# Kernel optimization log

Measured on AMD Instinct MI355X. Metric: run time of the kernel, lower is better.

The kernel has to match this reference:

```python
import math
import jax, jax.numpy as jnp
import numpy as np

H = 4            # num_attention_heads
EPS = 1e-5       # InstanceNorm / LayerNorm eps (torch default)


def _inorm(x):
    # nn.InstanceNorm1d applied to (N, S, d): normalizes over the last dim per (item, token), no affine
    m = jnp.mean(x, axis=-1, keepdims=True)
    v = jnp.var(x, axis=-1, keepdims=True)
    return (x - m) / jnp.sqrt(v + EPS)


def _tree_layer(x, Wqkv, bqkv, Wo, bo, W1, b1, W2, b2):
    # x: (N, S, d) with S=2
    N, S, d = x.shape
    dh = d // H
    qkv = x @ Wqkv.T + bqkv                      # (N, S, 3d)
    q, k, v = jnp.split(qkv, 3, axis=-1)
    q = q.reshape(N, S, H, dh)
    k = k.reshape(N, S, H, dh)
    v = v.reshape(N, S, H, dh)
    scores = jnp.einsum('nqhd,nkhd->nhqk', q, k) / math.sqrt(dh)
    att = jax.nn.softmax(scores, axis=-1)
    o = jnp.einsum('nhqk,nkhd->nqhd', att, v).reshape(N, S, d)
    o = o @ Wo.T + bo
    x = _inorm(x + o)
    f = jax.nn.gelu(x @ W1.T + b1, approximate=False) @ W2.T + b2
    return _inorm(x + f)


def _mlp(x, Wa, ba, Wb, bb):
    return jax.nn.gelu(x @ Wa.T + ba, approximate=False) @ Wb.T + bb


def setup_inputs() -> dict:
    key = jax.random.key(0)
    ks = jax.random.split(key, 16)
    B, G, d, ff, L, c = 64, 1024, 256, 1024, 4, 128
    s = 0.02
    r = lambda i, shape: (jax.random.normal(ks[i], shape, jnp.float32) * s)
    return dict(
        children=jax.random.normal(ks[0], (B, G, 2, d), jnp.float32),
        roles=r(1, (3, d)),
        Wqkv=r(2, (L, 3 * d, d)), bqkv=jnp.zeros((L, 3 * d), jnp.float32),
        Wo=r(3, (L, d, d)), bo=jnp.zeros((L, d), jnp.float32),
        W1=r(4, (L, ff, d)), b1=jnp.zeros((L, ff), jnp.float32),
        W2=r(5, (L, d, ff)), b2=jnp.zeros((L, d), jnp.float32),
        Wl1=r(6, (d, d)), bl1=jnp.zeros(d, jnp.float32),
        Wl2=r(7, (c, d)), bl2=jnp.zeros(c, jnp.float32),
        Wr1=r(8, (d, d)), br1=jnp.zeros(d, jnp.float32),
        Wr2=r(9, (c, d)), br2=jnp.zeros(c, jnp.float32),
        ln_g=jnp.ones(d, jnp.float32), ln_b=jnp.zeros(d, jnp.float32),
    )


def reference(children, roles, Wqkv, bqkv, Wo, bo, W1, b1, W2, b2,
              Wl1, bl1, Wl2, bl2, Wr1, br1, Wr2, br2, ln_g, ln_b):
    B, G, _, d = children.shape
    c = Wl2.shape[0]
    L = Wqkv.shape[0]
    # flatten (batch, group) and add inside role embeddings (rows 0,1)
    x = children.reshape(B * G, 2, d) + roles[:2][None, :, :]
    for i in range(L):
        x = _tree_layer(x, Wqkv[i], bqkv[i], Wo[i], bo[i], W1[i], b1[i], W2[i], b2[i])
    out = x.reshape(B, G, 2, d)
    left_const = _mlp(out[:, :, 0, :], Wl1, bl1, Wl2, bl2)   # (B, G, c)
    right_const = _mlp(out[:, :, 1, :], Wr1, br1, Wr2, br2)  # (B, G, c)
    mat_scores = jnp.sum(left_const * right_const, axis=-1) / math.sqrt(c)
    # LayerNorm over last dim of summed children
    s = out.sum(axis=2)
    m = jnp.mean(s, axis=-1, keepdims=True)
    v = jnp.var(s, axis=-1, keepdims=True)
    src = (s - m) / jnp.sqrt(v + EPS) * ln_g + ln_b
    return mat_scores, src
```

## Files before the change

### kernel.cpp

```cpp
#include <hip/hip_runtime.h>
#include <math.h>

#define NLAYER 4
#define DMODEL 256
#define ITEMS  32
#define MROWS  64
#define XS     264
#define BS     520
#define EPSV   1e-5f

typedef __attribute__((ext_vector_type(8))) short short8;
typedef __attribute__((ext_vector_type(4))) float f32x4;

#define OFF_WQKV 0
#define OFF_WO   786432
#define OFF_W1   1048576
#define OFF_W2   2097152
#define OFF_WL1  3145728
#define OFF_WL2  3211264
#define OFF_WR1  3244032
#define OFF_WR2  3309568
#define WS_ELEMS 3342336

static __device__ __forceinline__ float b2f(short s) {
  return __uint_as_float(((unsigned)(unsigned short)s) << 16);
}
static __device__ __forceinline__ short f2bf(float f) {
  unsigned u = __float_as_uint(f);
  return (short)((u + 0x7fffu + ((u >> 16) & 1u)) >> 16);
}
static __device__ __forceinline__ float gelu_f(float x) {
  return 0.5f * x * (1.0f + erff(x * 0.70710678118654752f));
}

template<int MT>
static __device__ void gemm_lds(const short* A, int as, int rmul, int radd,
                                const short* __restrict__ W,
                                const float* __restrict__ bias,
                                short* Out, int oc0, int oro,
                                int N, int act, int tid)
{
  const int wave = tid >> 6;
  const int lane = tid & 63;
  const int lm = lane & 15;
  const int q  = lane >> 4;
  const int ntiles = N >> 4;
  const f32x4 z = {0.f, 0.f, 0.f, 0.f};
  for (int nb = wave * 2; nb < ntiles; nb += 16) {
    f32x4 acc[MT][2];
    #pragma unroll
    for (int mt = 0; mt < MT; ++mt) { acc[mt][0] = z; acc[mt][1] = z; }
    #pragma unroll 4
    for (int kt = 0; kt < 256; kt += 32) {
      short8 b0 = *(const short8*)(W + ((nb    ) * 16 + lm) * 256 + kt + q * 8);
      short8 b1 = *(const short8*)(W + ((nb + 1) * 16 + lm) * 256 + kt + q * 8);
      #pragma unroll
      for (int mt = 0; mt < MT; ++mt) {
        short8 a = *(const short8*)(A + (rmul * (mt * 16 + lm) + radd) * as + kt + q * 8);
        acc[mt][0] = __builtin_amdgcn_mfma_f32_16x16x32_bf16(a, b0, acc[mt][0], 0, 0, 0);
        acc[mt][1] = __builtin_amdgcn_mfma_f32_16x16x32_bf16(a, b1, acc[mt][1], 0, 0, 0);
      }
    }
    #pragma unroll
    for (int mt = 0; mt < MT; ++mt) {
      #pragma unroll
      for (int nt = 0; nt < 2; ++nt) {
        int col = (nb + nt) * 16 + lm;
        float bv = bias[col];
        #pragma unroll
        for (int r = 0; r < 4; ++r) {
          float v = acc[mt][nt][r] + bv;
          if (act) v = gelu_f(v);
          Out[(oro + mt * 16 + q * 4 + r) * BS + oc0 + col] = f2bf(v);
        }
      }
    }
  }
}

static __device__ void gemm_acc512(f32x4 acc[4][2], const short* A,
                                   const short* __restrict__ W, int wc0, int tid)
{
  const int wave = tid >> 6, lane = tid & 63;
  const int lm = lane & 15, q = lane >> 4;
  #pragma unroll 2
  for (int kt = 0; kt < 512; kt += 32) {
    short8 b[2];
    #pragma unroll
    for (int nt = 0; nt < 2; ++nt)
      b[nt] = *(const short8*)(W + (wave * 32 + nt * 16 + lm) * 1024 + wc0 + kt + q * 8);
    #pragma unroll
    for (int mt = 0; mt < 4; ++mt) {
      short8 a = *(const short8*)(A + (mt * 16 + lm) * BS + kt + q * 8);
      #pragma unroll
      for (int nt = 0; nt < 2; ++nt)
        acc[mt][nt] = __builtin_amdgcn_mfma_f32_16x16x32_bf16(a, b[nt], acc[mt][nt], 0, 0, 0);
    }
  }
}

static __device__ void inorm_pass(short* Xs_, const short* Bf_, bool addx, int tid)
{
  if (tid >= MROWS * 4) return;
  int r = tid >> 2, sub = tid & 3;
  const short* bp = Bf_ + r * BS + sub * 64;
  short* xp = Xs_ + r * XS + sub * 64;
  float sum = 0.f, sq = 0.f;
  for (int e = 0; e < 64; ++e) {
    float v = b2f(bp[e]);
    if (addx) v += b2f(xp[e]);
    sum += v; sq += v * v;
  }
  sum += __shfl_xor(sum, 1); sq += __shfl_xor(sq, 1);
  sum += __shfl_xor(sum, 2); sq += __shfl_xor(sq, 2);
  float mean = sum * (1.f / 256.f);
  float rstd = rsqrtf(sq * (1.f / 256.f) - mean * mean + EPSV);
  for (int e = 0; e < 64; ++e) {
    float v = b2f(bp[e]);
    if (addx) v += b2f(xp[e]);
    xp[e] = f2bf((v - mean) * rstd);
  }
}

struct PrepArgs {
  const float* src[8];
  int n[8];
  int off[8];
};

__global__ void prep_weights(PrepArgs pa, short* __restrict__ dst, int total)
{
  int idx = blockIdx.x * 256 + threadIdx.x;
  if (idx >= total) return;
  int j = 0, off = idx;
  while (j < 7 && off >= pa.n[j]) { off -= pa.n[j]; ++j; }
  dst[pa.off[j] + off] = f2bf(pa.src[j][off]);
}

__global__ __launch_bounds__(512, 2)
void fused_encoder(const float* __restrict__ children,
                   const float* __restrict__ roles,
                   const short* __restrict__ ws,
                   const float* __restrict__ g_bqkv,
                   const float* __restrict__ g_bo,
                   const float* __restrict__ g_b1,
                   const float* __restrict__ g_b2,
                   const float* __restrict__ g_bl1, const float* __restrict__ g_bl2,
                   const float* __restrict__ g_br1, const float* __restrict__ g_br2,
                   const float* __restrict__ g_lng, const float* __restrict__ g_lnb,
                   float* __restrict__ out)
{
  __shared__ __align__(16) short Xs[MROWS * XS];
  __shared__ __align__(16) short Bf[MROWS * BS];
  __shared__ float Att[ITEMS * 16];

  const int tid = threadIdx.x;
  const int bid = blockIdx.x;

  {
    const float* src = children + (long)bid * MROWS * DMODEL;
    for (int e = tid * 4; e < MROWS * DMODEL; e += 2048) {
      int row = e >> 8, col = e & 255;
      float4 v = *(const float4*)(src + e);
      const float* rl = roles + (row & 1) * DMODEL + col;
      short* xp = Xs + row * XS + col;
      xp[0] = f2bf(v.x + rl[0]);
      xp[1] = f2bf(v.y + rl[1]);
      xp[2] = f2bf(v.z + rl[2]);
      xp[3] = f2bf(v.w + rl[3]);
    }
  }
  __syncthreads();

  for (int l = 0; l < NLAYER; ++l) {
    const short* Wqkv = ws + OFF_WQKV + l * 768 * 256;
    const short* Wo   = ws + OFF_WO   + l * 256 * 256;
    const short* W1   = ws + OFF_W1   + l * 1024 * 256;
    const short* W2   = ws + OFF_W2   + l * 256 * 1024;

    gemm_lds<4>(Xs, XS, 1, 0, Wqkv, g_bqkv + l * 768, Bf, 0, 0, 512, 0, tid);
    __syncthreads();

    if (tid < ITEMS * 8) {
      int i = tid >> 3, h = (tid >> 1) & 3, tk = tid & 1;
      const short* qp = Bf + (2 * i + tk) * BS + h * 64;
      const short* k0 = Bf + (2 * i    ) * BS + 256 + h * 64;
      const short* k1 = Bf + (2 * i + 1) * BS + 256 + h * 64;
      float s0 = 0.f, s1 = 0.f;
      for (int e = 0; e < 64; ++e) {
        float qv = b2f(qp[e]);
        s0 += qv * b2f(k0[e]);
        s1 += qv * b2f(k1[e]);
      }
      s0 *= 0.125f; s1 *= 0.125f;
      float mx = fmaxf(s0, s1);
      float e0 = __expf(s0 - mx), e1 = __expf(s1 - mx);
      float inv = 1.f / (e0 + e1);
      float* ap = Att + ((i * 4 + h) * 2 + tk) * 2;
      ap[0] = e0 * inv; ap[1] = e1 * inv;
    }
    __syncthreads();

    gemm_lds<4>(Xs, XS, 1, 0, Wqkv + 512 * 256, g_bqkv + l * 768 + 512, Bf, 0, 0, 256, 0, tid);
    __syncthreads();

    if (tid < MROWS * 4) {
      int r = tid >> 2, h = tid & 3;
      int i = r >> 1, tk = r & 1;
      const float* ap = Att + ((i * 4 + h) * 2 + tk) * 2;
      float a0 = ap[0], a1 = ap[1];
      const short* v0 = Bf + (2 * i) * BS + h * 64;
      const short* v1 = Bf + (2 * i + 1) * BS + h * 64;
      short* op = Bf + r * BS + 256 + h * 64;
      for (int e = 0; e < 64; ++e)
        op[e] = f2bf(a0 * b2f(v0[e]) + a1 * b2f(v1[e]));
    }
    __syncthreads();

    gemm_lds<4>(Bf + 256, BS, 1, 0, Wo, g_bo + l * 256, Bf, 0, 0, 256, 0, tid);
    __syncthreads();
    inorm_pass(Xs, Bf, true, tid);
    __syncthreads();

    f32x4 facc[4][2];
    {
      const f32x4 z = {0.f, 0.f, 0.f, 0.f};
      #pragma unroll
      for (int mt = 0; mt < 4; ++mt) { facc[mt][0] = z; facc[mt][1] = z; }
    }
    for (int ch = 0; ch < 2; ++ch) {
      gemm_lds<4>(Xs, XS, 1, 0, W1 + ch * 512 * 256, g_b1 + l * 1024 + ch * 512,
                  Bf, 0, 0, 512, 1, tid);
      __syncthreads();
      gemm_acc512(facc, Bf, W2, ch * 512, tid);
      __syncthreads();
    }
    {
      const int wave = tid >> 6, lane = tid & 63, lm = lane & 15, q = lane >> 4;
      #pragma unroll
      for (int mt = 0; mt < 4; ++mt)
        #pragma unroll
        for (int nt = 0; nt < 2; ++nt) {
          int col = wave * 32 + nt * 16 + lm;
          float bv = g_b2[l * 256 + col];
          #pragma unroll
          for (int r = 0; r < 4; ++r) {
            int row = mt * 16 + q * 4 + r;
            Bf[row * BS + col] = f2bf(facc[mt][nt][r] + bv + b2f(Xs[row * XS + col]));
          }
        }
    }
    __syncthreads();
    inorm_pass(Xs, Bf, false, tid);
    __syncthreads();
  }

  gemm_lds<2>(Xs, XS, 2, 0, ws + OFF_WL1, g_bl1, Bf, 0, 0, 256, 1, tid);
  gemm_lds<2>(Xs, XS, 2, 1, ws + OFF_WR1, g_br1, Bf, 256, 0, 256, 1, tid);
  __syncthreads();
  gemm_lds<2>(Bf, BS, 1, 0, ws + OFF_WL2, g_bl2, Bf, 0, 32, 128, 0, tid);
  gemm_lds<2>(Bf + 256, BS, 1, 0, ws + OFF_WR2, g_br2, Bf, 128, 32, 128, 0, tid);
  __syncthreads();

  if (tid < ITEMS * 8) {
    int i = tid >> 3, sub = tid & 7;
    const short* lp = Bf + (32 + i) * BS + sub * 16;
    float acc = 0.f;
    for (int j = 0; j < 16; ++j) acc += b2f(lp[j]) * b2f(lp[128 + j]);
    acc += __shfl_xor(acc, 1);
    acc += __shfl_xor(acc, 2);
    acc += __shfl_xor(acc, 4);
    if (sub == 0) out[bid * ITEMS + i] = acc * 0.088388347648318447f;
  }
  if (tid < ITEMS * 8) {
    int i = tid >> 3, sub = tid & 7;
    const short* x0 = Xs + (2 * i) * XS + sub * 32;
    const short* x1 = Xs + (2 * i + 1) * XS + sub * 32;
    float sum = 0.f, sq = 0.f;
    for (int e = 0; e < 32; ++e) {
      float v = b2f(x0[e]) + b2f(x1[e]);
      sum += v; sq += v * v;
    }
    sum += __shfl_xor(sum, 1); sq += __shfl_xor(sq, 1);
    sum += __shfl_xor(sum, 2); sq += __shfl_xor(sq, 2);
    sum += __shfl_xor(sum, 4); sq += __shfl_xor(sq, 4);
    float mean = sum * (1.f / 256.f);
    float rstd = rsqrtf(sq * (1.f / 256.f) - mean * mean + EPSV);
    float* op = out + 65536 + ((long)bid * ITEMS + i) * DMODEL + sub * 32;
    for (int e = 0; e < 32; ++e) {
      int c = sub * 32 + e;
      float v = b2f(x0[e]) + b2f(x1[e]);
      op[e] = (v - mean) * rstd * g_lng[c] + g_lnb[c];
    }
  }
}

extern "C" void kernel_launch(void* const* d_in, const int* in_sizes, int n_in,
                              void* d_out, int out_size, void* d_ws, size_t ws_size,
                              hipStream_t stream)
{
  (void)in_sizes; (void)n_in; (void)out_size; (void)ws_size;
  const float* children = (const float*)d_in[0];
  const float* roles    = (const float*)d_in[1];
  const float* Wqkv     = (const float*)d_in[2];
  const float* bqkv     = (const float*)d_in[3];
  const float* Wo       = (const float*)d_in[4];
  const float* bo       = (const float*)d_in[5];
  const float* W1       = (const float*)d_in[6];
  const float* b1       = (const float*)d_in[7];
  const float* W2       = (const float*)d_in[8];
  const float* b2       = (const float*)d_in[9];
  const float* Wl1      = (const float*)d_in[10];
  const float* bl1      = (const float*)d_in[11];
  const float* Wl2      = (const float*)d_in[12];
  const float* bl2      = (const float*)d_in[13];
  const float* Wr1      = (const float*)d_in[14];
  const float* br1      = (const float*)d_in[15];
  const float* Wr2      = (const float*)d_in[16];
  const float* br2      = (const float*)d_in[17];
  const float* ln_g     = (const float*)d_in[18];
  const float* ln_b     = (const float*)d_in[19];

  short* ws = (short*)d_ws;

  PrepArgs pa;
  pa.src[0] = Wqkv; pa.n[0] = 786432;  pa.off[0] = OFF_WQKV;
  pa.src[1] = Wo;   pa.n[1] = 262144;  pa.off[1] = OFF_WO;
  pa.src[2] = W1;   pa.n[2] = 1048576; pa.off[2] = OFF_W1;
  pa.src[3] = W2;   pa.n[3] = 1048576; pa.off[3] = OFF_W2;
  pa.src[4] = Wl1;  pa.n[4] = 65536;   pa.off[4] = OFF_WL1;
  pa.src[5] = Wl2;  pa.n[5] = 32768;   pa.off[5] = OFF_WL2;
  pa.src[6] = Wr1;  pa.n[6] = 65536;   pa.off[6] = OFF_WR1;
  pa.src[7] = Wr2;  pa.n[7] = 32768;   pa.off[7] = OFF_WR2;

  prep_weights<<<(WS_ELEMS + 255) / 256, 256, 0, stream>>>(pa, ws, WS_ELEMS);
  fused_encoder<<<2048, 512, 0, stream>>>(children, roles, ws,
      bqkv, bo, b1, b2, bl1, bl2, br1, br2, ln_g, ln_b, (float*)d_out);
}
```

Before: 2.685 ms.

## Double block size to 16 waves and redistribute GEMM column tiles per wave

The fused encoder moves from 512 to 1024 threads per block, and the GEMM helpers are templated on how many 16-column tiles each wave owns. Waves now take one tile each where the 256-wide outputs previously needed two per wave. The goal is more waves per block to hide MFMA and global weight-load latency, with fewer accumulators per wave. In exchange, the launch bounds drop the two-blocks-per-CU hint, so occupancy may shift. Each wave also reuses its A fragments across fewer tiles, which means more LDS traffic per MFMA.

```diff
diff --git a/kernel.cpp b/kernel.cpp
--- a/kernel.cpp
+++ b/kernel.cpp
@@ -8,6 +8,7 @@
 #define XS     264
 #define BS     520
 #define EPSV   1e-5f
+#define NWAVES 16
 
 typedef __attribute__((ext_vector_type(8))) short short8;
 typedef __attribute__((ext_vector_type(4))) float f32x4;
@@ -33,7 +34,7 @@
   return 0.5f * x * (1.0f + erff(x * 0.70710678118654752f));
 }
 
-template<int MT>
+template<int MT, int PAIR>
 static __device__ void gemm_lds(const short* A, int as, int rmul, int radd,
                                 const short* __restrict__ W,
                                 const float* __restrict__ bias,
@@ -46,30 +47,35 @@
   const int q  = lane >> 4;
   const int ntiles = N >> 4;
   const f32x4 z = {0.f, 0.f, 0.f, 0.f};
-  for (int nb = wave * 2; nb < ntiles; nb += 16) {
-    f32x4 acc[MT][2];
+  for (int nb = wave * PAIR; nb < ntiles; nb += NWAVES * PAIR) {
+    f32x4 acc[MT][PAIR];
     #pragma unroll
-    for (int mt = 0; mt < MT; ++mt) { acc[mt][0] = z; acc[mt][1] = z; }
+    for (int mt = 0; mt < MT; ++mt)
+      #pragma unroll
+      for (int p = 0; p < PAIR; ++p) acc[mt][p] = z;
     #pragma unroll 4
     for (int kt = 0; kt < 256; kt += 32) {
-      short8 b0 = *(const short8*)(W + ((nb    ) * 16 + lm) * 256 + kt + q * 8);
-      short8 b1 = *(const short8*)(W + ((nb + 1) * 16 + lm) * 256 + kt + q * 8);
+      short8 b[PAIR];
+      #pragma unroll
+      for (int p = 0; p < PAIR; ++p)
+        b[p] = *(const short8*)(W + ((nb + p) * 16 + lm) * 256 + kt + q * 8);
       #pragma unroll
       for (int mt = 0; mt < MT; ++mt) {
         short8 a = *(const short8*)(A + (rmul * (mt * 16 + lm) + radd) * as + kt + q * 8);
-        acc[mt][0] = __builtin_amdgcn_mfma_f32_16x16x32_bf16(a, b0, acc[mt][0], 0, 0, 0);
-        acc[mt][1] = __builtin_amdgcn_mfma_f32_16x16x32_bf16(a, b1, acc[mt][1], 0, 0, 0);
+        #pragma unroll
+        for (int p = 0; p < PAIR; ++p)
+          acc[mt][p] = __builtin_amdgcn_mfma_f32_16x16x32_bf16(a, b[p], acc[mt][p], 0, 0, 0);
       }
     }
     #pragma unroll
     for (int mt = 0; mt < MT; ++mt) {
       #pragma unroll
-      for (int nt = 0; nt < 2; ++nt) {
-        int col = (nb + nt) * 16 + lm;
+      for (int p = 0; p < PAIR; ++p) {
+        int col = (nb + p) * 16 + lm;
         float bv = bias[col];
         #pragma unroll
         for (int r = 0; r < 4; ++r) {
-          float v = acc[mt][nt][r] + bv;
+          float v = acc[mt][p][r] + bv;
           if (act) v = gelu_f(v);
           Out[(oro + mt * 16 + q * 4 + r) * BS + oc0 + col] = f2bf(v);
         }
@@ -78,23 +84,18 @@
   }
 }
 
-static __device__ void gemm_acc512(f32x4 acc[4][2], const short* A,
+static __device__ void gemm_acc512(f32x4 acc[4], const short* A,
                                    const short* __restrict__ W, int wc0, int tid)
 {
   const int wave = tid >> 6, lane = tid & 63;
   const int lm = lane & 15, q = lane >> 4;
   #pragma unroll 2
   for (int kt = 0; kt < 512; kt += 32) {
-    short8 b[2];
-    #pragma unroll
-    for (int nt = 0; nt < 2; ++nt)
-      b[nt] = *(const short8*)(W + (wave * 32 + nt * 16 + lm) * 1024 + wc0 + kt + q * 8);
+    short8 b = *(const short8*)(W + (wave * 16 + lm) * 1024 + wc0 + kt + q * 8);
     #pragma unroll
     for (int mt = 0; mt < 4; ++mt) {
       short8 a = *(const short8*)(A + (mt * 16 + lm) * BS + kt + q * 8);
-      #pragma unroll
-      for (int nt = 0; nt < 2; ++nt)
-        acc[mt][nt] = __builtin_amdgcn_mfma_f32_16x16x32_bf16(a, b[nt], acc[mt][nt], 0, 0, 0);
+      acc[mt] = __builtin_amdgcn_mfma_f32_16x16x32_bf16(a, b, acc[mt], 0, 0, 0);
     }
   }
 }
@@ -137,7 +138,7 @@
   dst[pa.off[j] + off] = f2bf(pa.src[j][off]);
 }
 
-__global__ __launch_bounds__(512, 2)
+__global__ __launch_bounds__(1024)
 void fused_encoder(const float* __restrict__ children,
                    const float* __restrict__ roles,
                    const short* __restrict__ ws,
@@ -159,7 +160,7 @@
 
   {
     const float* src = children + (long)bid * MROWS * DMODEL;
-    for (int e = tid * 4; e < MROWS * DMODEL; e += 2048) {
+    for (int e = tid * 4; e < MROWS * DMODEL; e += 4096) {
       int row = e >> 8, col = e & 255;
       float4 v = *(const float4*)(src + e);
       const float* rl = roles + (row & 1) * DMODEL + col;
@@ -178,7 +179,7 @@
     const short* W1   = ws + OFF_W1   + l * 1024 * 256;
     const short* W2   = ws + OFF_W2   + l * 256 * 1024;
 
-    gemm_lds<4>(Xs, XS, 1, 0, Wqkv, g_bqkv + l * 768, Bf, 0, 0, 512, 0, tid);
+    gemm_lds<4, 2>(Xs, XS, 1, 0, Wqkv, g_bqkv + l * 768, Bf, 0, 0, 512, 0, tid);
     __syncthreads();
 
     if (tid < ITEMS * 8) {
@@ -201,7 +202,7 @@
     }
     __syncthreads();
 
-    gemm_lds<4>(Xs, XS, 1, 0, Wqkv + 512 * 256, g_bqkv + l * 768 + 512, Bf, 0, 0, 256, 0, tid);
+    gemm_lds<4, 1>(Xs, XS, 1, 0, Wqkv + 512 * 256, g_bqkv + l * 768 + 512, Bf, 0, 0, 256, 0, tid);
     __syncthreads();
 
     if (tid < MROWS * 4) {
@@ -217,49 +218,47 @@
     }
     __syncthreads();
 
-    gemm_lds<4>(Bf + 256, BS, 1, 0, Wo, g_bo + l * 256, Bf, 0, 0, 256, 0, tid);
+    gemm_lds<4, 1>(Bf + 256, BS, 1, 0, Wo, g_bo + l * 256, Bf, 0, 0, 256, 0, tid);
     __syncthreads();
     inorm_pass(Xs, Bf, true, tid);
     __syncthreads();
 
-    f32x4 facc[4][2];
+    f32x4 facc[4];
     {
       const f32x4 z = {0.f, 0.f, 0.f, 0.f};
       #pragma unroll
-      for (int mt = 0; mt < 4; ++mt) { facc[mt][0] = z; facc[mt][1] = z; }
+      for (int mt = 0; mt < 4; ++mt) facc[mt] = z;
     }
     for (int ch = 0; ch < 2; ++ch) {
-      gemm_lds<4>(Xs, XS, 1, 0, W1 + ch * 512 * 256, g_b1 + l * 1024 + ch * 512,
-                  Bf, 0, 0, 512, 1, tid);
+      gemm_lds<4, 2>(Xs, XS, 1, 0, W1 + ch * 512 * 256, g_b1 + l * 1024 + ch * 512,
+                     Bf, 0, 0, 512, 1, tid);
       __syncthreads();
       gemm_acc512(facc, Bf, W2, ch * 512, tid);
       __syncthreads();
     }
     {
       const int wave = tid >> 6, lane = tid & 63, lm = lane & 15, q = lane >> 4;
-      #pragma unroll
-      for (int mt = 0; mt < 4; ++mt)
+      int col = wave * 16 + lm;
+      float bv = g_b2[l * 256 + col];
+      #pragma unroll
+      for (int mt = 0; mt < 4; ++mt) {
         #pragma unroll
-        for (int nt = 0; nt < 2; ++nt) {
-          int col = wave * 32 + nt * 16 + lm;
-          float bv = g_b2[l * 256 + col];
-          #pragma unroll
-          for (int r = 0; r < 4; ++r) {
-            int row = mt * 16 + q * 4 + r;
-            Bf[row * BS + col] = f2bf(facc[mt][nt][r] + bv + b2f(Xs[row * XS + col]));
-          }
+        for (int r = 0; r < 4; ++r) {
+          int row = mt * 16 + q * 4 + r;
+          Bf[row * BS + col] = f2bf(facc[mt][r] + bv + b2f(Xs[row * XS + col]));
         }
+      }
     }
     __syncthreads();
     inorm_pass(Xs, Bf, false, tid);
     __syncthreads();
   }
 
-  gemm_lds<2>(Xs, XS, 2, 0, ws + OFF_WL1, g_bl1, Bf, 0, 0, 256, 1, tid);
-  gemm_lds<2>(Xs, XS, 2, 1, ws + OFF_WR1, g_br1, Bf, 256, 0, 256, 1, tid);
+  gemm_lds<2, 1>(Xs, XS, 2, 0, ws + OFF_WL1, g_bl1, Bf, 0, 0, 256, 1, tid);
+  gemm_lds<2, 1>(Xs, XS, 2, 1, ws + OFF_WR1, g_br1, Bf, 256, 0, 256, 1, tid);
   __syncthreads();
-  gemm_lds<2>(Bf, BS, 1, 0, ws + OFF_WL2, g_bl2, Bf, 0, 32, 128, 0, tid);
-  gemm_lds<2>(Bf + 256, BS, 1, 0, ws + OFF_WR2, g_br2, Bf, 128, 32, 128, 0, tid);
+  gemm_lds<2, 1>(Bf, BS, 1, 0, ws + OFF_WL2, g_bl2, Bf, 0, 32, 128, 0, tid);
+  gemm_lds<2, 1>(Bf + 256, BS, 1, 0, ws + OFF_WR2, g_br2, Bf, 128, 32, 128, 0, tid);
   __syncthreads();
 
   if (tid < ITEMS * 8) {
@@ -334,6 +333,6 @@
   pa.src[7] = Wr2;  pa.n[7] = 32768;   pa.off[7] = OFF_WR2;
 
   prep_weights<<<(WS_ELEMS + 255) / 256, 256, 0, stream>>>(pa, ws, WS_ELEMS);
-  fused_encoder<<<2048, 512, 0, stream>>>(children, roles, ws,
+  fused_encoder<<<2048, 1024, 0, stream>>>(children, roles, ws,
       bqkv, bo, b1, b2, bl1, bl2, br1, br2, ln_g, ln_b, (float*)d_out);
 }
```

Result: faster. 2.416 ms (-10.0%).
